# Kernel tuning notes

Measured on AMD Instinct MI355X. Metric: run time of the kernel, lower is better.

The kernel has to match this reference:

```python
import jax, jax.numpy as jnp
import numpy as np

EMBED_DIM = 512
NUM_HEADS = 8
HEAD_DIM = EMBED_DIM // NUM_HEADS


def setup_inputs() -> dict:
    key = jax.random.key(0)
    ks = jax.random.split(key, 9)
    d = EMBED_DIM
    s = 1.0 / np.sqrt(d)
    inp = {
        "x": jax.random.normal(ks[0], (2, 4096, d), dtype=jnp.float32),
        # torch nn.Linear weights are [out, in]; we store them the same way
        "Wq": jax.random.uniform(ks[1], (d, d), jnp.float32, -s, s),
        "bq": jax.random.uniform(ks[2], (d,), jnp.float32, -s, s),
        "Wk": jax.random.uniform(ks[3], (d, d), jnp.float32, -s, s),
        "bk": jax.random.uniform(ks[4], (d,), jnp.float32, -s, s),
        "Wv": jax.random.uniform(ks[5], (d, d), jnp.float32, -s, s),
        "bv": jax.random.uniform(ks[6], (d,), jnp.float32, -s, s),
        "Wo": jax.random.uniform(ks[7], (d, d), jnp.float32, -s, s),
        "bo": jax.random.uniform(ks[8], (d,), jnp.float32, -s, s),
    }
    return inp


def reference(x, Wq, bq, Wk, bk, Wv, bv, Wo, bo):
    B, S, D = x.shape
    H, Hd = NUM_HEADS, HEAD_DIM

    def proj(W, b):  # torch Linear: x @ W.T + b
        y = jnp.einsum("bsd,ed->bse", x, W) + b
        return y.reshape(B, S, H, Hd).transpose(0, 2, 1, 3)  # [B,H,S,Hd]

    Q = proj(Wq, bq)
    K = proj(Wk, bk)
    V = proj(Wv, bv)

    scale = 1.0 / jnp.sqrt(jnp.float32(Hd))
    scores = jnp.einsum("bhqd,bhkd->bhqk", Q, K) * scale  # [B,H,S,S]
    attn = jax.nn.softmax(scores, axis=-1)
    out = jnp.einsum("bhqk,bhkd->bhqd", attn, V)  # [B,H,S,Hd]
    out = out.transpose(0, 2, 1, 3).reshape(B, S, D)
    return jnp.einsum("bsd,ed->bse", out, Wo) + bo
```

## Files before the change

### kernel.cpp

```cpp
#include <hip/hip_runtime.h>


typedef unsigned short ushortT;
typedef __attribute__((ext_vector_type(8))) short short8;
typedef __attribute__((ext_vector_type(4))) float f32x4;
typedef __attribute__((ext_vector_type(16))) float f32x16;
typedef __attribute__((ext_vector_type(4))) unsigned int uint4v;
typedef __attribute__((ext_vector_type(2))) unsigned int uint2v;

__device__ __forceinline__ ushortT f2bf(float f) {
    unsigned int u = __builtin_bit_cast(unsigned int, f);
    u += 0x7FFFu + ((u >> 16) & 1u);
    return (ushortT)(u >> 16);
}

__device__ __forceinline__ unsigned int cvtpk(float lo, float hi) {
    unsigned int d;
    asm("v_cvt_pk_bf16_f32 %0, %1, %2" : "=v"(d) : "v"(lo), "v"(hi));
    return d;
}

__device__ __forceinline__ uint4v pk8(f32x4 a0, f32x4 a1) {
    uint4v r = { cvtpk(a0[0], a0[1]), cvtpk(a0[2], a0[3]),
                 cvtpk(a1[0], a1[1]), cvtpk(a1[2], a1[3]) };
    return r;
}

__device__ __forceinline__ void plswap(unsigned int &a, unsigned int &b) {
    uint2v r = __builtin_amdgcn_permlane32_swap(a, b, false, false);
    a = r[0]; b = r[1];
}

#define GLDA 40
#define ALDK 72

__global__ __launch_bounds__(256) void proj_qkv(
    const float* __restrict__ x,
    const float* __restrict__ Wq, const float* __restrict__ bq,
    const float* __restrict__ Wk, const float* __restrict__ bk,
    const float* __restrict__ Wv, const float* __restrict__ bv,
    ushortT* __restrict__ Qw, ushortT* __restrict__ Kw,
    ushortT* __restrict__ Vtw, float qscale)
{
    __shared__ __align__(16) ushortT As[128 * GLDA];
    __shared__ __align__(16) ushortT Bs[128 * GLDA];
    const int t = threadIdx.x;
    const int w = t >> 6, lane = t & 63;
    const int quad = lane >> 4, l15 = lane & 15;
    const int z = blockIdx.z;
    const int bx = blockIdx.x, by = blockIdx.y;
    const int wm = (w >> 1) * 64, wn = (w & 1) * 64;

    const float* W    = (z == 0) ? Wq : (z == 1) ? Wk : Wv;
    const float* bias = (z == 0) ? bq : (z == 1) ? bk : bv;
    const float* Asrc = (z < 2) ? x : W;
    const float* Bsrc = (z < 2) ? W : x;
    const int arow0 = (z < 2) ? bx * 128 : by * 128;
    const int brow0 = (z < 2) ? by * 128 : bx * 128;

    const int sr0 = t >> 2, sc0 = (t & 3) * 8;
    const int sr1 = (t + 256) >> 2, sc1 = ((t + 256) & 3) * 8;

    f32x4 pa[2][2], pb[2][2];
    {
        const float* ap0 = Asrc + (size_t)(arow0 + sr0) * 512 + sc0;
        const float* ap1 = Asrc + (size_t)(arow0 + sr1) * 512 + sc1;
        const float* bp0 = Bsrc + (size_t)(brow0 + sr0) * 512 + sc0;
        const float* bp1 = Bsrc + (size_t)(brow0 + sr1) * 512 + sc1;
        pa[0][0] = *(const f32x4*)ap0; pa[0][1] = *(const f32x4*)(ap0 + 4);
        pa[1][0] = *(const f32x4*)ap1; pa[1][1] = *(const f32x4*)(ap1 + 4);
        pb[0][0] = *(const f32x4*)bp0; pb[0][1] = *(const f32x4*)(bp0 + 4);
        pb[1][0] = *(const f32x4*)bp1; pb[1][1] = *(const f32x4*)(bp1 + 4);
    }

    f32x4 acc[4][4] = {};

    for (int k0 = 0; k0 < 512; k0 += 32) {
        *(uint4v*)(As + sr0 * GLDA + sc0) = pk8(pa[0][0], pa[0][1]);
        *(uint4v*)(As + sr1 * GLDA + sc1) = pk8(pa[1][0], pa[1][1]);
        *(uint4v*)(Bs + sr0 * GLDA + sc0) = pk8(pb[0][0], pb[0][1]);
        *(uint4v*)(Bs + sr1 * GLDA + sc1) = pk8(pb[1][0], pb[1][1]);
        __syncthreads();

        if (k0 < 480) {
            const int kn = k0 + 32;
            const float* ap0 = Asrc + (size_t)(arow0 + sr0) * 512 + kn + sc0;
            const float* ap1 = Asrc + (size_t)(arow0 + sr1) * 512 + kn + sc1;
            const float* bp0 = Bsrc + (size_t)(brow0 + sr0) * 512 + kn + sc0;
            const float* bp1 = Bsrc + (size_t)(brow0 + sr1) * 512 + kn + sc1;
            pa[0][0] = *(const f32x4*)ap0; pa[0][1] = *(const f32x4*)(ap0 + 4);
            pa[1][0] = *(const f32x4*)ap1; pa[1][1] = *(const f32x4*)(ap1 + 4);
            pb[0][0] = *(const f32x4*)bp0; pb[0][1] = *(const f32x4*)(bp0 + 4);
            pb[1][0] = *(const f32x4*)bp1; pb[1][1] = *(const f32x4*)(bp1 + 4);
        }

        short8 af[4], bfr[4];
#pragma unroll
        for (int i = 0; i < 4; i++)
            af[i] = *(const short8*)(As + (wm + i * 16 + l15) * GLDA + quad * 8);
#pragma unroll
        for (int i = 0; i < 4; i++)
            bfr[i] = *(const short8*)(Bs + (wn + i * 16 + l15) * GLDA + quad * 8);
#pragma unroll
        for (int mi = 0; mi < 4; mi++)
#pragma unroll
            for (int ni = 0; ni < 4; ni++)
                acc[mi][ni] = __builtin_amdgcn_mfma_f32_16x16x32_bf16(
                    af[mi], bfr[ni], acc[mi][ni], 0, 0, 0);
        __syncthreads();
    }

    if (z < 2) {
        ushortT* Y = (z == 0) ? Qw : Kw;
        const float sc = (z == 0) ? qscale : 1.0f;
#pragma unroll
        for (int ni = 0; ni < 4; ni++) {
            int col = brow0 + wn + ni * 16 + l15;
            float bv_ = bias[col];
#pragma unroll
            for (int mi = 0; mi < 4; mi++)
#pragma unroll
                for (int r = 0; r < 4; r++) {
                    int row = arow0 + wm + mi * 16 + quad * 4 + r;
                    Y[(size_t)row * 512 + col] = f2bf((acc[mi][ni][r] + bv_) * sc);
                }
        }
    } else {
        const int bidx = brow0 >> 12;
        const int s0 = brow0 & 4095;
#pragma unroll
        for (int mi = 0; mi < 4; mi++)
#pragma unroll
            for (int r = 0; r < 4; r++) {
                int ch = arow0 + wm + mi * 16 + quad * 4 + r;
                float bv_ = bias[ch];
#pragma unroll
                for (int ni = 0; ni < 4; ni++) {
                    int s = s0 + wn + ni * 16 + l15;
                    Vtw[(size_t)bidx * 2097152 + (size_t)ch * 4096 + s] =
                        f2bf(acc[mi][ni][r] + bv_);
                }
            }
    }
}

__global__ __launch_bounds__(256) void gemm_out(
    const ushortT* __restrict__ X, const float* __restrict__ W,
    const float* __restrict__ bias, float* __restrict__ Y)
{
    __shared__ __align__(16) ushortT As[128 * GLDA];
    __shared__ __align__(16) ushortT Bs[128 * GLDA];
    const int t = threadIdx.x;
    const int w = t >> 6, lane = t & 63;
    const int quad = lane >> 4, l15 = lane & 15;
    const int bm = blockIdx.x * 128, bn = blockIdx.y * 128;
    const int wm = (w >> 1) * 64, wn = (w & 1) * 64;

    const int sr0 = t >> 2, sc0 = (t & 3) * 8;
    const int sr1 = (t + 256) >> 2, sc1 = ((t + 256) & 3) * 8;

    uint4v pa[2];
    f32x4 pb[2][2];
    {
        pa[0] = *(const uint4v*)(X + (size_t)(bm + sr0) * 512 + sc0);
        pa[1] = *(const uint4v*)(X + (size_t)(bm + sr1) * 512 + sc1);
        const float* bp0 = W + (size_t)(bn + sr0) * 512 + sc0;
        const float* bp1 = W + (size_t)(bn + sr1) * 512 + sc1;
        pb[0][0] = *(const f32x4*)bp0; pb[0][1] = *(const f32x4*)(bp0 + 4);
        pb[1][0] = *(const f32x4*)bp1; pb[1][1] = *(const f32x4*)(bp1 + 4);
    }

    f32x4 acc[4][4] = {};

    for (int k0 = 0; k0 < 512; k0 += 32) {
        *(uint4v*)(As + sr0 * GLDA + sc0) = pa[0];
        *(uint4v*)(As + sr1 * GLDA + sc1) = pa[1];
        *(uint4v*)(Bs + sr0 * GLDA + sc0) = pk8(pb[0][0], pb[0][1]);
        *(uint4v*)(Bs + sr1 * GLDA + sc1) = pk8(pb[1][0], pb[1][1]);
        __syncthreads();

        if (k0 < 480) {
            const int kn = k0 + 32;
            pa[0] = *(const uint4v*)(X + (size_t)(bm + sr0) * 512 + kn + sc0);
            pa[1] = *(const uint4v*)(X + (size_t)(bm + sr1) * 512 + kn + sc1);
            const float* bp0 = W + (size_t)(bn + sr0) * 512 + kn + sc0;
            const float* bp1 = W + (size_t)(bn + sr1) * 512 + kn + sc1;
            pb[0][0] = *(const f32x4*)bp0; pb[0][1] = *(const f32x4*)(bp0 + 4);
            pb[1][0] = *(const f32x4*)bp1; pb[1][1] = *(const f32x4*)(bp1 + 4);
        }

        short8 af[4], bfr[4];
#pragma unroll
        for (int i = 0; i < 4; i++)
            af[i] = *(const short8*)(As + (wm + i * 16 + l15) * GLDA + quad * 8);
#pragma unroll
        for (int i = 0; i < 4; i++)
            bfr[i] = *(const short8*)(Bs + (wn + i * 16 + l15) * GLDA + quad * 8);
#pragma unroll
        for (int mi = 0; mi < 4; mi++)
#pragma unroll
            for (int ni = 0; ni < 4; ni++)
                acc[mi][ni] = __builtin_amdgcn_mfma_f32_16x16x32_bf16(
                    af[mi], bfr[ni], acc[mi][ni], 0, 0, 0);
        __syncthreads();
    }

#pragma unroll
    for (int ni = 0; ni < 4; ni++) {
        int col = bn + wn + ni * 16 + l15;
        float bv = bias[col];
#pragma unroll
        for (int mi = 0; mi < 4; mi++)
#pragma unroll
            for (int r = 0; r < 4; r++) {
                int row = bm + wm + mi * 16 + quad * 4 + r;
                Y[(size_t)row * 512 + col] = acc[mi][ni][r] + bv;
            }
    }
}

__device__ __forceinline__ void softmax_pack(const f32x16 &sacc, float &lp,
                                             uint4v &B0, uint4v &B1)
{
    float p[16];
#pragma unroll
    for (int r = 0; r < 16; r++) {
        p[r] = __builtin_amdgcn_exp2f(sacc[r]);
        lp += p[r];
    }
    unsigned int c00 = cvtpk(p[0],  p[1]),  c01 = cvtpk(p[2],  p[3]);
    unsigned int c10 = cvtpk(p[4],  p[5]),  c11 = cvtpk(p[6],  p[7]);
    unsigned int c20 = cvtpk(p[8],  p[9]),  c21 = cvtpk(p[10], p[11]);
    unsigned int c30 = cvtpk(p[12], p[13]), c31 = cvtpk(p[14], p[15]);
    plswap(c00, c10);
    plswap(c01, c11);
    plswap(c20, c30);
    plswap(c21, c31);
    B0 = uint4v{ c00, c01, c10, c11 };
    B1 = uint4v{ c20, c21, c30, c31 };
}

__global__ __launch_bounds__(512, 2) void attn(
    const ushortT* Q, const ushortT* __restrict__ K,
    const ushortT* __restrict__ Vt, ushortT* O)
{
    __shared__ __align__(16) ushortT SM[2][2][2][64 * ALDK];

    const int t = threadIdx.x;
    const int w = t >> 6, lane = t & 63;
    const int half = w >> 2, qw = w & 3;
    const int l31 = lane & 31, hh = lane >> 5;

    const int j = blockIdx.x + (blockIdx.y << 4);
    const int qt = (j >> 3) & 15;
    const int bh = ((j & 7) << 1) | (j >> 7);

    const int b = bh >> 3, h = bh & 7;
    const size_t qbase = (size_t)b * 4096 + qt * 256 + qw * 64;

    short8 qf[2][4];
#pragma unroll
    for (int qg = 0; qg < 2; qg++) {
        const ushortT* qp = Q + (qbase + qg * 32 + l31) * 512 + h * 64 + hh * 8;
#pragma unroll
        for (int dk = 0; dk < 4; dk++)
            qf[qg][dk] = *(const short8*)(qp + dk * 16);
    }

    f32x16 oacc[2][2] = {};
    float lpart[2] = {};

    const int kofs = half * 2048;
    const ushortT* Kbase = K + ((size_t)b * 4096 + kofs) * 512 + h * 64;
    const ushortT* Vbase = Vt + (size_t)b * 2097152 + (size_t)h * 64 * 4096 + kofs;

    const int th = t & 255;
    const int srow = th >> 3, scol = (th & 7) * 8;
    uint4v kg[2], vg[2];

#pragma unroll
    for (int i = 0; i < 2; i++) {
        kg[i] = *(const uint4v*)(Kbase + (size_t)(srow + 32 * i) * 512 + scol);
        vg[i] = *(const uint4v*)(Vbase + (size_t)(srow + 32 * i) * 4096 + scol);
    }
#pragma unroll
    for (int i = 0; i < 2; i++) {
        *(uint4v*)(SM[0][half][0] + (srow + 32 * i) * ALDK + scol) = kg[i];
        *(uint4v*)(SM[1][half][0] + (srow + 32 * i) * ALDK + scol) = vg[i];
    }
    __syncthreads();

    for (int kt = 0; kt < 32; kt++) {
        const int cur = kt & 1;

        if (kt < 31) {
            const int kb = (kt + 1) * 64;
#pragma unroll
            for (int i = 0; i < 2; i++) {
                kg[i] = *(const uint4v*)(Kbase + (size_t)(kb + srow + 32 * i) * 512 + scol);
                vg[i] = *(const uint4v*)(Vbase + (size_t)(srow + 32 * i) * 4096 + kb + scol);
            }
        }

        const ushortT* Kt  = SM[0][half][cur];
        const ushortT* Vtl = SM[1][half][cur];

#pragma unroll
        for (int st = 0; st < 2; st++) {
            short8 kf[4];
#pragma unroll
            for (int dk = 0; dk < 4; dk++)
                kf[dk] = *(const short8*)(Kt + (st * 32 + l31) * ALDK + dk * 16 + hh * 8);
            f32x16 s0 = {}, s1 = {};
#pragma unroll
            for (int dk = 0; dk < 4; dk++) {
                s0 = __builtin_amdgcn_mfma_f32_32x32x16_bf16(kf[dk], qf[0][dk], s0, 0, 0, 0);
                s1 = __builtin_amdgcn_mfma_f32_32x32x16_bf16(kf[dk], qf[1][dk], s1, 0, 0, 0);
            }

            uint4v B00, B01, B10, B11;
            softmax_pack(s0, lpart[0], B00, B01);
            softmax_pack(s1, lpart[1], B10, B11);
            short8 p00 = __builtin_bit_cast(short8, B00);
            short8 p01 = __builtin_bit_cast(short8, B01);
            short8 p10 = __builtin_bit_cast(short8, B10);
            short8 p11 = __builtin_bit_cast(short8, B11);

#pragma unroll
            for (int dt = 0; dt < 2; dt++) {
                short8 vf0 = *(const short8*)(Vtl + (dt * 32 + l31) * ALDK + st * 32 + hh * 8);
                short8 vf1 = *(const short8*)(Vtl + (dt * 32 + l31) * ALDK + st * 32 + 16 + hh * 8);
                oacc[0][dt] = __builtin_amdgcn_mfma_f32_32x32x16_bf16(vf0, p00, oacc[0][dt], 0, 0, 0);
                oacc[0][dt] = __builtin_amdgcn_mfma_f32_32x32x16_bf16(vf1, p01, oacc[0][dt], 0, 0, 0);
                oacc[1][dt] = __builtin_amdgcn_mfma_f32_32x32x16_bf16(vf0, p10, oacc[1][dt], 0, 0, 0);
                oacc[1][dt] = __builtin_amdgcn_mfma_f32_32x32x16_bf16(vf1, p11, oacc[1][dt], 0, 0, 0);
            }
        }

        if (kt < 31) {
            const int nb = cur ^ 1;
#pragma unroll
            for (int i = 0; i < 2; i++) {
                *(uint4v*)(SM[0][half][nb] + (srow + 32 * i) * ALDK + scol) = kg[i];
                *(uint4v*)(SM[1][half][nb] + (srow + 32 * i) * ALDK + scol) = vg[i];
            }
        }
        __syncthreads();
    }

    float* scratch = (float*)&SM[0][0][0][0];
    float* prow = scratch + (size_t)(qw * 64 + lane) * 68;

    if (half == 1) {
#pragma unroll
        for (int qg = 0; qg < 2; qg++)
#pragma unroll
            for (int dt = 0; dt < 2; dt++)
#pragma unroll
                for (int m = 0; m < 4; m++) {
                    f32x4 v4 = { oacc[qg][dt][4 * m + 0], oacc[qg][dt][4 * m + 1],
                                 oacc[qg][dt][4 * m + 2], oacc[qg][dt][4 * m + 3] };
                    *(f32x4*)(prow + qg * 32 + dt * 16 + m * 4) = v4;
                }
        prow[64] = lpart[0];
        prow[65] = lpart[1];
    }
    __syncthreads();

    if (half == 0) {
#pragma unroll
        for (int qg = 0; qg < 2; qg++) {
            float sum = lpart[qg] + prow[64 + qg];
            float l = sum + __shfl_xor(sum, 32);
            float rl = 1.0f / l;

            ushortT* orow = O + (qbase + qg * 32 + l31) * 512 + h * 64 + hh * 4;
#pragma unroll
            for (int dt = 0; dt < 2; dt++)
#pragma unroll
                for (int m = 0; m < 4; m++) {
                    f32x4 v4 = *(const f32x4*)(prow + qg * 32 + dt * 16 + m * 4);
                    unsigned int u0 = cvtpk((oacc[qg][dt][4 * m + 0] + v4[0]) * rl,
                                            (oacc[qg][dt][4 * m + 1] + v4[1]) * rl);
                    unsigned int u1 = cvtpk((oacc[qg][dt][4 * m + 2] + v4[2]) * rl,
                                            (oacc[qg][dt][4 * m + 3] + v4[3]) * rl);
                    uint2v st2 = { u0, u1 };
                    *(uint2v*)(orow + dt * 32 + m * 8) = st2;
                }
        }
    }
}

extern "C" void kernel_launch(void* const* d_in, const int* in_sizes, int n_in,
                              void* d_out, int out_size, void* d_ws, size_t ws_size,
                              hipStream_t stream)
{
    const float* x  = (const float*)d_in[0];
    const float* Wq = (const float*)d_in[1];
    const float* bq = (const float*)d_in[2];
    const float* Wk = (const float*)d_in[3];
    const float* bk = (const float*)d_in[4];
    const float* Wv = (const float*)d_in[5];
    const float* bv = (const float*)d_in[6];
    const float* Wo = (const float*)d_in[7];
    const float* bo = (const float*)d_in[8];

    ushortT* ws  = (ushortT*)d_ws;
    ushortT* Qw  = ws;
    ushortT* Kw  = ws + 4194304;
    ushortT* Vtw = ws + 2 * 4194304;

    const float qscale = 0.125f * 1.44269504089f;

    proj_qkv<<<dim3(64, 4, 3), 256, 0, stream>>>(
        x, Wq, bq, Wk, bk, Wv, bv, Qw, Kw, Vtw, qscale);
    attn<<<dim3(16, 16), 512, 0, stream>>>(Qw, Kw, Vtw, Qw);
    gemm_out<<<dim3(64, 4), 256, 0, stream>>>(Qw, Wo, bo, (float*)d_out);
}
```

Before: 193.9 us.

## Pre-convert inputs to bf16 and stage GEMM tiles via direct global-to-LDS loads

Adds a prep kernel that converts x and all four weight matrices to bf16 once. The projection and output GEMMs then load bf16 tiles straight into LDS with global_load_lds, which removes the register prefetch and the in-loop packing. The V projection is recast as x·Wv^T with a packed transposed store instead of a W·x^T product. The cost is an extra kernel launch, an extra pass over memory, an unpadded LDS layout that may cause bank conflicts, and the loss of the register double-buffering prefetch.

```diff
diff --git a/kernel.cpp b/kernel.cpp
--- a/kernel.cpp
+++ b/kernel.cpp
@@ -31,76 +31,78 @@
     a = r[0]; b = r[1];
 }
 
-#define GLDA 40
+__device__ __forceinline__ void gload16(const ushortT* g, ushortT* l) {
+    __builtin_amdgcn_global_load_lds(
+        (const __attribute__((address_space(1))) void*)g,
+        (__attribute__((address_space(3))) void*)l, 16, 0, 0);
+}
+
 #define ALDK 72
 
+__global__ __launch_bounds__(256) void prep(
+    const float* __restrict__ x,  const float* __restrict__ Wq,
+    const float* __restrict__ Wk, const float* __restrict__ Wv,
+    const float* __restrict__ Wo,
+    ushortT* __restrict__ xb, ushortT* __restrict__ wb)
+{
+    const int bid = blockIdx.x, t = threadIdx.x;
+    const float* src; ushortT* dst; size_t base;
+    if (bid < 2048) { src = x; dst = xb; base = (size_t)bid * 2048; }
+    else {
+        int r = bid - 2048, wsel = r >> 7, rb = r & 127;
+        src = (wsel == 0) ? Wq : (wsel == 1) ? Wk : (wsel == 2) ? Wv : Wo;
+        dst = wb + (size_t)wsel * 262144;
+        base = (size_t)rb * 2048;
+    }
+    const size_t off = base + (size_t)t * 8;
+    f32x4 a0 = *(const f32x4*)(src + off);
+    f32x4 a1 = *(const f32x4*)(src + off + 4);
+    *(uint4v*)(dst + off) = pk8(a0, a1);
+}
+
 __global__ __launch_bounds__(256) void proj_qkv(
-    const float* __restrict__ x,
-    const float* __restrict__ Wq, const float* __restrict__ bq,
-    const float* __restrict__ Wk, const float* __restrict__ bk,
-    const float* __restrict__ Wv, const float* __restrict__ bv,
+    const ushortT* __restrict__ xb, const ushortT* __restrict__ wb,
+    const float* __restrict__ bq, const float* __restrict__ bk,
+    const float* __restrict__ bv,
     ushortT* __restrict__ Qw, ushortT* __restrict__ Kw,
     ushortT* __restrict__ Vtw, float qscale)
 {
-    __shared__ __align__(16) ushortT As[128 * GLDA];
-    __shared__ __align__(16) ushortT Bs[128 * GLDA];
+    __shared__ __align__(16) ushortT As[128 * 32];
+    __shared__ __align__(16) ushortT Bs[128 * 32];
     const int t = threadIdx.x;
     const int w = t >> 6, lane = t & 63;
     const int quad = lane >> 4, l15 = lane & 15;
     const int z = blockIdx.z;
-    const int bx = blockIdx.x, by = blockIdx.y;
+    const int arow0 = blockIdx.x * 128;
+    const int brow0 = blockIdx.y * 128;
     const int wm = (w >> 1) * 64, wn = (w & 1) * 64;
 
-    const float* W    = (z == 0) ? Wq : (z == 1) ? Wk : Wv;
+    const ushortT* Wz = wb + (size_t)z * 262144;
     const float* bias = (z == 0) ? bq : (z == 1) ? bk : bv;
-    const float* Asrc = (z < 2) ? x : W;
-    const float* Bsrc = (z < 2) ? W : x;
-    const int arow0 = (z < 2) ? bx * 128 : by * 128;
-    const int brow0 = (z < 2) ? by * 128 : bx * 128;
-
-    const int sr0 = t >> 2, sc0 = (t & 3) * 8;
-    const int sr1 = (t + 256) >> 2, sc1 = ((t + 256) & 3) * 8;
-
-    f32x4 pa[2][2], pb[2][2];
-    {
-        const float* ap0 = Asrc + (size_t)(arow0 + sr0) * 512 + sc0;
-        const float* ap1 = Asrc + (size_t)(arow0 + sr1) * 512 + sc1;
-        const float* bp0 = Bsrc + (size_t)(brow0 + sr0) * 512 + sc0;
-        const float* bp1 = Bsrc + (size_t)(brow0 + sr1) * 512 + sc1;
-        pa[0][0] = *(const f32x4*)ap0; pa[0][1] = *(const f32x4*)(ap0 + 4);
-        pa[1][0] = *(const f32x4*)ap1; pa[1][1] = *(const f32x4*)(ap1 + 4);
-        pb[0][0] = *(const f32x4*)bp0; pb[0][1] = *(const f32x4*)(bp0 + 4);
-        pb[1][0] = *(const f32x4*)bp1; pb[1][1] = *(const f32x4*)(bp1 + 4);
-    }
+
+    const int srow = lane >> 2;
+    const int scol = (lane & 3) * 8;
+    ushortT* Ad0 = As + (w * 2 + 0) * 512;
+    ushortT* Ad1 = As + (w * 2 + 1) * 512;
+    ushortT* Bd0 = Bs + (w * 2 + 0) * 512;
+    ushortT* Bd1 = Bs + (w * 2 + 1) * 512;
 
     f32x4 acc[4][4] = {};
 
     for (int k0 = 0; k0 < 512; k0 += 32) {
-        *(uint4v*)(As + sr0 * GLDA + sc0) = pk8(pa[0][0], pa[0][1]);
-        *(uint4v*)(As + sr1 * GLDA + sc1) = pk8(pa[1][0], pa[1][1]);
-        *(uint4v*)(Bs + sr0 * GLDA + sc0) = pk8(pb[0][0], pb[0][1]);
-        *(uint4v*)(Bs + sr1 * GLDA + sc1) = pk8(pb[1][0], pb[1][1]);
+        gload16(xb + (size_t)(arow0 + w * 32 +      srow) * 512 + k0 + scol, Ad0);
+        gload16(xb + (size_t)(arow0 + w * 32 + 16 + srow) * 512 + k0 + scol, Ad1);
+        gload16(Wz + (size_t)(brow0 + w * 32 +      srow) * 512 + k0 + scol, Bd0);
+        gload16(Wz + (size_t)(brow0 + w * 32 + 16 + srow) * 512 + k0 + scol, Bd1);
         __syncthreads();
 
-        if (k0 < 480) {
-            const int kn = k0 + 32;
-            const float* ap0 = Asrc + (size_t)(arow0 + sr0) * 512 + kn + sc0;
-            const float* ap1 = Asrc + (size_t)(arow0 + sr1) * 512 + kn + sc1;
-            const float* bp0 = Bsrc + (size_t)(brow0 + sr0) * 512 + kn + sc0;
-            const float* bp1 = Bsrc + (size_t)(brow0 + sr1) * 512 + kn + sc1;
-            pa[0][0] = *(const f32x4*)ap0; pa[0][1] = *(const f32x4*)(ap0 + 4);
-            pa[1][0] = *(const f32x4*)ap1; pa[1][1] = *(const f32x4*)(ap1 + 4);
-            pb[0][0] = *(const f32x4*)bp0; pb[0][1] = *(const f32x4*)(bp0 + 4);
-            pb[1][0] = *(const f32x4*)bp1; pb[1][1] = *(const f32x4*)(bp1 + 4);
-        }
-
         short8 af[4], bfr[4];
 #pragma unroll
         for (int i = 0; i < 4; i++)
-            af[i] = *(const short8*)(As + (wm + i * 16 + l15) * GLDA + quad * 8);
+            af[i] = *(const short8*)(As + (wm + i * 16 + l15) * 32 + quad * 8);
 #pragma unroll
         for (int i = 0; i < 4; i++)
-            bfr[i] = *(const short8*)(Bs + (wn + i * 16 + l15) * GLDA + quad * 8);
+            bfr[i] = *(const short8*)(Bs + (wn + i * 16 + l15) * 32 + quad * 8);
 #pragma unroll
         for (int mi = 0; mi < 4; mi++)
 #pragma unroll
@@ -126,76 +128,60 @@
                 }
         }
     } else {
-        const int bidx = brow0 >> 12;
-        const int s0 = brow0 & 4095;
-#pragma unroll
-        for (int mi = 0; mi < 4; mi++)
-#pragma unroll
-            for (int r = 0; r < 4; r++) {
-                int ch = arow0 + wm + mi * 16 + quad * 4 + r;
-                float bv_ = bias[ch];
-#pragma unroll
-                for (int ni = 0; ni < 4; ni++) {
-                    int s = s0 + wn + ni * 16 + l15;
-                    Vtw[(size_t)bidx * 2097152 + (size_t)ch * 4096 + s] =
-                        f2bf(acc[mi][ni][r] + bv_);
-                }
-            }
+        const int bidx = arow0 >> 12;
+        const int s0 = (arow0 & 4095) + wm;
+#pragma unroll
+        for (int ni = 0; ni < 4; ni++) {
+            int ch = brow0 + wn + ni * 16 + l15;
+            float bv_ = bias[ch];
+            ushortT* vrow = Vtw + (size_t)bidx * 2097152 + (size_t)ch * 4096;
+#pragma unroll
+            for (int mi = 0; mi < 4; mi++) {
+                int s = s0 + mi * 16 + quad * 4;
+                unsigned int u0 = cvtpk(acc[mi][ni][0] + bv_, acc[mi][ni][1] + bv_);
+                unsigned int u1 = cvtpk(acc[mi][ni][2] + bv_, acc[mi][ni][3] + bv_);
+                uint2v st2 = { u0, u1 };
+                *(uint2v*)(vrow + s) = st2;
+            }
+        }
     }
 }
 
 __global__ __launch_bounds__(256) void gemm_out(
-    const ushortT* __restrict__ X, const float* __restrict__ W,
+    const ushortT* __restrict__ X, const ushortT* __restrict__ Wob,
     const float* __restrict__ bias, float* __restrict__ Y)
 {
-    __shared__ __align__(16) ushortT As[128 * GLDA];
-    __shared__ __align__(16) ushortT Bs[128 * GLDA];
+    __shared__ __align__(16) ushortT As[128 * 32];
+    __shared__ __align__(16) ushortT Bs[128 * 32];
     const int t = threadIdx.x;
     const int w = t >> 6, lane = t & 63;
     const int quad = lane >> 4, l15 = lane & 15;
     const int bm = blockIdx.x * 128, bn = blockIdx.y * 128;
     const int wm = (w >> 1) * 64, wn = (w & 1) * 64;
 
-    const int sr0 = t >> 2, sc0 = (t & 3) * 8;
-    const int sr1 = (t + 256) >> 2, sc1 = ((t + 256) & 3) * 8;
-
-    uint4v pa[2];
-    f32x4 pb[2][2];
-    {
-        pa[0] = *(const uint4v*)(X + (size_t)(bm + sr0) * 512 + sc0);
-        pa[1] = *(const uint4v*)(X + (size_t)(bm + sr1) * 512 + sc1);
-        const float* bp0 = W + (size_t)(bn + sr0) * 512 + sc0;
-        const float* bp1 = W + (size_t)(bn + sr1) * 512 + sc1;
-        pb[0][0] = *(const f32x4*)bp0; pb[0][1] = *(const f32x4*)(bp0 + 4);
-        pb[1][0] = *(const f32x4*)bp1; pb[1][1] = *(const f32x4*)(bp1 + 4);
-    }
+    const int srow = lane >> 2;
+    const int scol = (lane & 3) * 8;
+    ushortT* Ad0 = As + (w * 2 + 0) * 512;
+    ushortT* Ad1 = As + (w * 2 + 1) * 512;
+    ushortT* Bd0 = Bs + (w * 2 + 0) * 512;
+    ushortT* Bd1 = Bs + (w * 2 + 1) * 512;
 
     f32x4 acc[4][4] = {};
 
     for (int k0 = 0; k0 < 512; k0 += 32) {
-        *(uint4v*)(As + sr0 * GLDA + sc0) = pa[0];
-        *(uint4v*)(As + sr1 * GLDA + sc1) = pa[1];
-        *(uint4v*)(Bs + sr0 * GLDA + sc0) = pk8(pb[0][0], pb[0][1]);
-        *(uint4v*)(Bs + sr1 * GLDA + sc1) = pk8(pb[1][0], pb[1][1]);
+        gload16(X   + (size_t)(bm + w * 32 +      srow) * 512 + k0 + scol, Ad0);
+        gload16(X   + (size_t)(bm + w * 32 + 16 + srow) * 512 + k0 + scol, Ad1);
+        gload16(Wob + (size_t)(bn + w * 32 +      srow) * 512 + k0 + scol, Bd0);
+        gload16(Wob + (size_t)(bn + w * 32 + 16 + srow) * 512 + k0 + scol, Bd1);
         __syncthreads();
 
-        if (k0 < 480) {
-            const int kn = k0 + 32;
-            pa[0] = *(const uint4v*)(X + (size_t)(bm + sr0) * 512 + kn + sc0);
-            pa[1] = *(const uint4v*)(X + (size_t)(bm + sr1) * 512 + kn + sc1);
-            const float* bp0 = W + (size_t)(bn + sr0) * 512 + kn + sc0;
-            const float* bp1 = W + (size_t)(bn + sr1) * 512 + kn + sc1;
-            pb[0][0] = *(const f32x4*)bp0; pb[0][1] = *(const f32x4*)(bp0 + 4);
-            pb[1][0] = *(const f32x4*)bp1; pb[1][1] = *(const f32x4*)(bp1 + 4);
-        }
-
         short8 af[4], bfr[4];
 #pragma unroll
         for (int i = 0; i < 4; i++)
-            af[i] = *(const short8*)(As + (wm + i * 16 + l15) * GLDA + quad * 8);
+            af[i] = *(const short8*)(As + (wm + i * 16 + l15) * 32 + quad * 8);
 #pragma unroll
         for (int i = 0; i < 4; i++)
-            bfr[i] = *(const short8*)(Bs + (wn + i * 16 + l15) * GLDA + quad * 8);
+            bfr[i] = *(const short8*)(Bs + (wn + i * 16 + l15) * 32 + quad * 8);
 #pragma unroll
         for (int mi = 0; mi < 4; mi++)
 #pragma unroll
@@ -408,12 +394,15 @@
     ushortT* ws  = (ushortT*)d_ws;
     ushortT* Qw  = ws;
     ushortT* Kw  = ws + 4194304;
-    ushortT* Vtw = ws + 2 * 4194304;
+    ushortT* Vtw = ws + 8388608;
+    ushortT* xb  = ws + 12582912;
+    ushortT* wbf = ws + 16777216;
 
     const float qscale = 0.125f * 1.44269504089f;
 
+    prep<<<dim3(2560), 256, 0, stream>>>(x, Wq, Wk, Wv, Wo, xb, wbf);
     proj_qkv<<<dim3(64, 4, 3), 256, 0, stream>>>(
-        x, Wq, bq, Wk, bk, Wv, bv, Qw, Kw, Vtw, qscale);
+        xb, wbf, bq, bk, bv, Qw, Kw, Vtw, qscale);
     attn<<<dim3(16, 16), 512, 0, stream>>>(Qw, Kw, Vtw, Qw);
-    gemm_out<<<dim3(64, 4), 256, 0, stream>>>(Qw, Wo, bo, (float*)d_out);
-}
+    gemm_out<<<dim3(64, 4), 256, 0, stream>>>(Qw, wbf + 786432, bo, (float*)d_out);
+}
```

Result: no change. 197.4 us (+1.8%).
